# Kernel tuning notes

Measured on AMD Instinct MI355X. Metric: run time of the kernel, lower is better.

Reference implementation:

```python
import jax, jax.numpy as jnp
import numpy as np

N, L, H, E = 4, 4096, 8, 64
CHUNK = 128  # chunk size for the blocked causal scan
EPS = 1e-6


def elu_feature_map(x):
    # phi(x) = elu(x) + 1 (default feature map of fast-transformers)
    return jax.nn.elu(x) + 1.0


def causal_dot_product(Q, K, V, chunk=CHUNK):
    """out[n,l,h,:] = sum_{s<=l} (Q[n,l,h,:].K[n,s,h,:]) * V[n,s,h,:].
    Chunked scan over the [E,M] KV state: O(N L H E M) without an [L,L] matrix."""
    n, l, h, e = Q.shape
    m = V.shape[-1]
    nc = l // chunk

    def to_chunks(x):
        # [n, l, h, d] -> [nc, n, h, chunk, d]
        return x.reshape(n, nc, chunk, h, x.shape[-1]).transpose(1, 0, 3, 2, 4)

    q, k, v = to_chunks(Q), to_chunks(K), to_chunks(V)
    tril = jnp.tril(jnp.ones((chunk, chunk), dtype=Q.dtype))

    def step(S, xs):  # S: [n, h, e, m] running sum of k v^T
        qc, kc, vc = xs  # [n, h, chunk, e/m]
        inter = jnp.einsum('nhce,nhem->nhcm', qc, S)
        attn = jnp.einsum('nhce,nhde->nhcd', qc, kc) * tril  # intra-chunk causal
        intra = jnp.einsum('nhcd,nhdm->nhcm', attn, vc)
        S = S + jnp.einsum('nhce,nhcm->nhem', kc, vc)
        return S, inter + intra

    S0 = jnp.zeros((n, h, e, m), dtype=Q.dtype)
    _, out = jax.lax.scan(step, S0, (q, k, v))  # [nc, n, h, chunk, m]
    return out.transpose(1, 0, 3, 2, 4).reshape(n, l, h, m)


def setup_inputs() -> dict:
    key = jax.random.key(0)
    k1, k2, k3 = jax.random.split(key, 3)
    return {
        'queries': jax.random.normal(k1, (N, L, H, E), jnp.float32),
        'keys': jax.random.normal(k2, (N, L, H, E), jnp.float32),
        'values': jax.random.normal(k3, (N, L, H, E), jnp.float32),
        'key_lengths': jnp.ones((N, L), jnp.float32),  # float length mask
    }


def reference(queries, keys, values, key_lengths):
    Q = elu_feature_map(queries)
    K = elu_feature_map(keys) * key_lengths[:, :, None, None]
    # denominator: Z[n,l,h] = 1 / (Q[n,l,h] . cumsum_s<=l K[n,s,h] + eps)
    Z = 1.0 / (jnp.einsum('nlhe,nlhe->nlh', Q, jnp.cumsum(K, axis=1)) + EPS)
    V_new = causal_dot_product(Q, K, values)
    return V_new * Z[:, :, :, None]
```

## Files before the change

### kernel.cpp

```cpp
#include <hip/hip_runtime.h>
#include <math.h>

#define NN 4
#define LL 4096
#define HH 8
#define EE 64
#define CHK 64
#define GSUP 4
#define NSUP 16
#define NH (NN*HH)
#define NBLK (NH*NSUP)
#define NCH64 (LL/CHK)
#define EPSF 1e-6f

typedef float f32x4 __attribute__((ext_vector_type(4)));
typedef __bf16 bf16x8 __attribute__((ext_vector_type(8)));
typedef __bf16 bf16x4 __attribute__((ext_vector_type(4)));

__device__ __forceinline__ float phi_map(float x) {
  return x > 0.0f ? x + 1.0f : __expf(x);
}

#define MFMA(a, b, c) __builtin_amdgcn_mfma_f32_16x16x32_bf16((a), (b), (c), 0, 0, 0)

__device__ __forceinline__ int swz64(int row, int d) {
  return row * 64 + (d & 7) + 8 * ((d >> 3) ^ ((row >> 2) & 7));
}
__device__ __forceinline__ int frag64(int row, int blk) {
  return row * 64 + 8 * (blk ^ ((row >> 2) & 7));
}

#define K1_ISSUE(J, BUF) { \
  const int l0i = (sc * GSUP + (J)) * CHK; \
  _Pragma("unroll") for (int it = 0; it < 4; ++it) { \
    int f = t + 256 * it; int d = f >> 4; int c4 = (f & 15) << 2; \
    size_t gb = (((size_t)n * LL + (size_t)(l0i + d)) * HH + h) * EE + c4; \
    pk[BUF][it] = *(const float4*)(Kg + gb); \
    pv[BUF][it] = *(const float4*)(Vg + gb); \
    pl[BUF][it] = KLg[n * LL + l0i + d]; } }

#define K1_STAGE(BUF) { \
  _Pragma("unroll") for (int it = 0; it < 4; ++it) { \
    int f = t + 256 * it; int d = f >> 4; int c4 = (f & 15) << 2; \
    float klr = pl[BUF][it]; float4 kk = pk[BUF][it]; float4 vv = pv[BUF][it]; \
    float ka[4] = {phi_map(kk.x) * klr, phi_map(kk.y) * klr, phi_map(kk.z) * klr, phi_map(kk.w) * klr}; \
    float va[4] = {vv.x, vv.y, vv.z, vv.w}; \
    _Pragma("unroll") for (int jj = 0; jj < 4; ++jj) { \
      sKt[BUF][swz64(c4 + jj, d)] = (__bf16)ka[jj]; \
      sVt[BUF][swz64(c4 + jj, d)] = (__bf16)va[jj]; } } }

__global__ __launch_bounds__(256, 2) void k_chunksums(
    const float* __restrict__ Kg, const float* __restrict__ Vg,
    const float* __restrict__ KLg, __bf16* __restrict__ ScG, __bf16* __restrict__ KscG)
{
  __shared__ __bf16 sKt[2][4096];
  __shared__ __bf16 sVt[2][4096];
  const int g = blockIdx.x;
  const int sc = g & (NSUP - 1);
  const int nh = g >> 4;
  const int h = nh % HH;
  const int n = nh / HH;
  const int t = threadIdx.x;
  const int w = t >> 6;
  const int lane = t & 63;
  const int lg = lane >> 4;
  const int li = lane & 15;
  const int arow = 16 * w + li;

  float4 pk[2][4], pv[2][4];
  float pl[2][4];

  K1_ISSUE(0, 0);
  K1_STAGE(0);

  f32x4 acc[4];
  #pragma unroll
  for (int nt = 0; nt < 4; ++nt) acc[nt] = (f32x4){0.f, 0.f, 0.f, 0.f};

  bf16x8 ones;
  #pragma unroll
  for (int i = 0; i < 8; ++i) ones[i] = (__bf16)1.0f;

  #pragma unroll
  for (int j = 0; j < GSUP; ++j) {
    if (j + 1 < GSUP) K1_ISSUE(j + 1, (j + 1) & 1);
    __syncthreads();

    bf16x8 bV0 = *(const bf16x8*)&sVt[j & 1][frag64(arow, lg)];
    bf16x8 bV1 = *(const bf16x8*)&sVt[j & 1][frag64(arow, 4 + lg)];

    f32x4 accK[4];
    #pragma unroll
    for (int nt = 0; nt < 4; ++nt) accK[nt] = (f32x4){0.f, 0.f, 0.f, 0.f};

    #pragma unroll
    for (int nt = 0; nt < 4; ++nt) {
      bf16x8 a0 = *(const bf16x8*)&sKt[j & 1][frag64(li + 16 * nt, lg)];
      bf16x8 a1 = *(const bf16x8*)&sKt[j & 1][frag64(li + 16 * nt, 4 + lg)];
      acc[nt] = MFMA(a0, bV0, acc[nt]);
      acc[nt] = MFMA(a1, bV1, acc[nt]);
      if (w == 0) {
        accK[nt] = MFMA(ones, a0, accK[nt]);
        accK[nt] = MFMA(ones, a1, accK[nt]);
      }
    }
    if (w == 0 && lg == 0) {
      #pragma unroll
      for (int nt = 0; nt < 4; ++nt)
        KscG[(size_t)(g * GSUP + j) * 64 + li + 16 * nt] = (__bf16)accK[nt][0];
    }
    if (j + 1 < GSUP) K1_STAGE((j + 1) & 1);
  }

  __bf16* sp = ScG + (size_t)g * 4096;
  #pragma unroll
  for (int nt = 0; nt < 4; ++nt) {
    bf16x4 sv;
    #pragma unroll
    for (int reg = 0; reg < 4; ++reg) sv[reg] = (__bf16)acc[nt][reg];
    *(bf16x4*)(sp + arow * 64 + 16 * nt + 4 * lg) = sv;
  }
}

__global__ __launch_bounds__(256) void k_prefix(
    __bf16* __restrict__ Sc, __bf16* __restrict__ Ksc)
{
  const int bid = blockIdx.x;
  const int t = threadIdx.x;
  if (bid < NH * 16) {
    const int nh = bid >> 4;
    const int strip = bid & 15;
    const int entry = strip * 256 + t;
    __bf16 v[NSUP];
    #pragma unroll
    for (int c = 0; c < NSUP; ++c)
      v[c] = Sc[((size_t)(nh * NSUP + c) << 12) + entry];
    float run = 0.0f;
    #pragma unroll
    for (int c = 0; c < NSUP; ++c) {
      Sc[((size_t)(nh * NSUP + c) << 12) + entry] = (__bf16)run;
      run += (float)v[c];
    }
  } else {
    const int idx = (bid - NH * 16) * 256 + t;
    const int nh = idx >> 6;
    const int e = idx & 63;
    __bf16 v[NCH64];
    #pragma unroll
    for (int c = 0; c < NCH64; ++c)
      v[c] = Ksc[((size_t)(nh * NCH64 + c) << 6) + e];
    float run = 0.0f;
    #pragma unroll
    for (int c = 0; c < NCH64; ++c) {
      Ksc[((size_t)(nh * NCH64 + c) << 6) + e] = (__bf16)run;
      run += (float)v[c];
    }
  }
}

#define P2_ISSUE(CC) { \
  const int l0i = (sc * GSUP + (CC)) * CHK; \
  _Pragma("unroll") for (int it = 0; it < 4; ++it) { \
    int f = t + 256 * it; int d = f >> 4; int c4 = (f & 15) << 2; \
    size_t gb = (((size_t)n * LL + (size_t)(l0i + d)) * HH + h) * EE + c4; \
    pk[it] = *(const float4*)(Kg + gb); \
    pv[it] = *(const float4*)(Vg + gb); \
    pl[it] = KLg[n * LL + l0i + d]; } \
  { const float* qr = Qg + (((size_t)n * LL + (size_t)(l0i + arow)) * HH + h) * EE; \
    pq[0] = *(const float4*)(qr + 8 * lg); \
    pq[1] = *(const float4*)(qr + 8 * lg + 4); \
    pq[2] = *(const float4*)(qr + 32 + 8 * lg); \
    pq[3] = *(const float4*)(qr + 32 + 8 * lg + 4); } }

#define P2_STAGE(QB) { \
  _Pragma("unroll") for (int it = 0; it < 4; ++it) { \
    int f = t + 256 * it; int d = f >> 4; int c4 = (f & 15) << 2; \
    float klr = pl[it]; float4 kk = pk[it]; float4 vv = pv[it]; \
    float ka[4] = {phi_map(kk.x) * klr, phi_map(kk.y) * klr, phi_map(kk.z) * klr, phi_map(kk.w) * klr}; \
    float va[4] = {vv.x, vv.y, vv.z, vv.w}; \
    bf16x4 kv4; \
    kv4[0] = (__bf16)ka[0]; kv4[1] = (__bf16)ka[1]; kv4[2] = (__bf16)ka[2]; kv4[3] = (__bf16)ka[3]; \
    *(bf16x4*)&sKe[QB][d * 64 + 8 * ((c4 >> 3) ^ ((d >> 2) & 7)) + (c4 & 7)] = kv4; \
    _Pragma("unroll") for (int jj = 0; jj < 4; ++jj) { \
      sKt[QB][swz64(c4 + jj, d)] = (__bf16)ka[jj]; \
      sVt[QB][swz64(c4 + jj, d)] = (__bf16)va[jj]; } } \
  { float4 q0 = pq[0], q1 = pq[1], q2 = pq[2], q3 = pq[3]; \
    bf16x8 a0, a1; \
    a0[0] = (__bf16)phi_map(q0.x); a0[1] = (__bf16)phi_map(q0.y); \
    a0[2] = (__bf16)phi_map(q0.z); a0[3] = (__bf16)phi_map(q0.w); \
    a0[4] = (__bf16)phi_map(q1.x); a0[5] = (__bf16)phi_map(q1.y); \
    a0[6] = (__bf16)phi_map(q1.z); a0[7] = (__bf16)phi_map(q1.w); \
    a1[0] = (__bf16)phi_map(q2.x); a1[1] = (__bf16)phi_map(q2.y); \
    a1[2] = (__bf16)phi_map(q2.z); a1[3] = (__bf16)phi_map(q2.w); \
    a1[4] = (__bf16)phi_map(q3.x); a1[5] = (__bf16)phi_map(q3.y); \
    a1[6] = (__bf16)phi_map(q3.z); a1[7] = (__bf16)phi_map(q3.w); \
    aQ[QB][0] = a0; aQ[QB][1] = a1; } }

__global__ __launch_bounds__(256, 2) void k_pass2(
    const float* __restrict__ Qg, const float* __restrict__ Kg,
    const float* __restrict__ Vg, const float* __restrict__ KLg,
    const __bf16* __restrict__ Sp, const __bf16* __restrict__ Ksp,
    float* __restrict__ Og)
{
  __shared__ __bf16 sKe[2][4096];
  __shared__ __bf16 sKt[2][4096];
  __shared__ __bf16 sVt[2][4096];
  __shared__ __bf16 sU[2][4096];
  __shared__ __bf16 sP[4][1024];

  const int g = blockIdx.x;
  const int sc = g & (NSUP - 1);
  const int nh = g >> 4;
  const int h = nh % HH;
  const int n = nh / HH;
  const int t = threadIdx.x;
  const int w = t >> 6;
  const int lane = t & 63;
  const int lg = lane >> 4;
  const int li = lane & 15;
  const int arow = 16 * w + li;

  float4 pk[4], pv[4], pq[4];
  float pl[4];
  bf16x8 aQ[2][2];

  {
    const bf16x8* sp8 = (const bf16x8*)(Sp + (size_t)g * 4096);
    bf16x8 s0 = sp8[2 * t];
    bf16x8 s1 = sp8[2 * t + 1];
    int m = t >> 2, eb = (t & 3) * 2;
    *(bf16x8*)&sU[0][frag64(m, eb)] = s0;
    *(bf16x8*)&sU[0][frag64(m, eb + 1)] = s1;
  }

  f32x4 accS[4];
  #pragma unroll
  for (int nt = 0; nt < 4; ++nt) {
    bf16x4 sv = *(const bf16x4*)(Sp + (size_t)g * 4096 + arow * 64 + 16 * nt + 4 * lg);
    #pragma unroll
    for (int reg = 0; reg < 4; ++reg) accS[nt][reg] = (float)sv[reg];
  }

  P2_ISSUE(0);
  P2_STAGE(0);

  #pragma unroll
  for (int cc = 0; cc < GSUP; ++cc) {
    const int cb = cc & 1, nb = cb ^ 1;
    __syncthreads();

    if (cc + 1 < GSUP) P2_ISSUE(cc + 1);

    bf16x8 aQ0 = aQ[cb][0], aQ1 = aQ[cb][1];

    f32x4 acc[4];
    #pragma unroll
    for (int nt = 0; nt < 4; ++nt) {
      acc[nt] = (f32x4){0.f, 0.f, 0.f, 0.f};
      bf16x8 aS0 = *(const bf16x8*)&sU[cb][frag64(li + 16 * nt, lg)];
      bf16x8 aS1 = *(const bf16x8*)&sU[cb][frag64(li + 16 * nt, 4 + lg)];
      acc[nt] = MFMA(aS0, aQ0, acc[nt]);
      acc[nt] = MFMA(aS1, aQ1, acc[nt]);
    }

    const __bf16* kb = Ksp + (size_t)(g * GSUP + cc) * 64;
    bf16x8 ks0 = *(const bf16x8*)(kb + 8 * lg);
    bf16x8 ks1 = *(const bf16x8*)(kb + 32 + 8 * lg);
    float dv = 0.0f;
    #pragma unroll
    for (int i = 0; i < 8; ++i) {
      dv += (float)aQ0[i] * (float)ks0[i];
      dv += (float)aQ1[i] * (float)ks1[i];
    }
    dv += __shfl_xor(dv, 16);
    dv += __shfl_xor(dv, 32);

    f32x4 at2[4];
    #pragma unroll
    for (int nt = 0; nt < 4; ++nt) at2[nt] = (f32x4){0.f, 0.f, 0.f, 0.f};
    for (int nt = 0; nt <= w; ++nt) {
      bf16x8 aK0 = *(const bf16x8*)&sKe[cb][frag64(li + 16 * nt, lg)];
      bf16x8 aK1 = *(const bf16x8*)&sKe[cb][frag64(li + 16 * nt, 4 + lg)];
      at2[nt] = MFMA(aK0, aQ0, at2[nt]);
      at2[nt] = MFMA(aK1, aQ1, at2[nt]);
    }

    float rs = 0.0f;
    #pragma unroll
    for (int nt = 0; nt < 4; ++nt) {
      bf16x4 pw;
      #pragma unroll
      for (int reg = 0; reg < 4; ++reg) {
        int kk = 16 * nt + 4 * lg + reg;
        float av = (kk <= arow) ? at2[nt][reg] : 0.0f;
        rs += av;
        pw[reg] = (__bf16)av;
      }
      *(bf16x4*)&sP[w][li * 64 + 8 * ((2 * nt + (lg >> 1)) ^ (li & 7)) + 4 * (lg & 1)] = pw;
    }
    rs += __shfl_xor(rs, 16);
    rs += __shfl_xor(rs, 32);

    {
      bf16x8 bP0 = *(const bf16x8*)&sP[w][li * 64 + 8 * (lg ^ (li & 7))];
      bf16x8 bP1 = *(const bf16x8*)&sP[w][li * 64 + 8 * ((4 + lg) ^ (li & 7))];
      #pragma unroll
      for (int nt = 0; nt < 4; ++nt) {
        bf16x8 aV0 = *(const bf16x8*)&sVt[cb][frag64(li + 16 * nt, lg)];
        bf16x8 aV1 = *(const bf16x8*)&sVt[cb][frag64(li + 16 * nt, 4 + lg)];
        acc[nt] = MFMA(aV0, bP0, acc[nt]);
        acc[nt] = MFMA(aV1, bP1, acc[nt]);
      }
    }

    const int l0 = (sc * GSUP + cc) * CHK;
    {
      float inv = 1.0f / (dv + rs + EPSF);
      size_t ob = (((size_t)n * LL + (size_t)(l0 + arow)) * HH + h) * EE;
      #pragma unroll
      for (int nt = 0; nt < 4; ++nt) {
        float4 o = make_float4(acc[nt][0] * inv, acc[nt][1] * inv,
                               acc[nt][2] * inv, acc[nt][3] * inv);
        *(float4*)(Og + ob + 16 * nt + 4 * lg) = o;
      }
    }

    if (cc + 1 < GSUP) {
      bf16x8 bV0 = *(const bf16x8*)&sVt[cb][frag64(arow, lg)];
      bf16x8 bV1 = *(const bf16x8*)&sVt[cb][frag64(arow, 4 + lg)];
      #pragma unroll
      for (int nt = 0; nt < 4; ++nt) {
        bf16x8 aKt0 = *(const bf16x8*)&sKt[cb][frag64(li + 16 * nt, lg)];
        bf16x8 aKt1 = *(const bf16x8*)&sKt[cb][frag64(li + 16 * nt, 4 + lg)];
        accS[nt] = MFMA(aKt0, bV0, accS[nt]);
        accS[nt] = MFMA(aKt1, bV1, accS[nt]);
        bf16x4 sw;
        #pragma unroll
        for (int reg = 0; reg < 4; ++reg) sw[reg] = (__bf16)accS[nt][reg];
        *(bf16x4*)&sU[nb][arow * 64 + 8 * ((2 * nt + (lg >> 1)) ^ ((arow >> 2) & 7)) + 4 * (lg & 1)] = sw;
      }
      P2_STAGE(nb);
    }
  }
}

extern "C" void kernel_launch(void* const* d_in, const int* in_sizes, int n_in,
                              void* d_out, int out_size, void* d_ws, size_t ws_size,
                              hipStream_t stream) {
  const float* Qg  = (const float*)d_in[0];
  const float* Kg  = (const float*)d_in[1];
  const float* Vg  = (const float*)d_in[2];
  const float* KLg = (const float*)d_in[3];
  float* Og = (float*)d_out;

  __bf16* Sc  = (__bf16*)d_ws;
  __bf16* Ksc = (__bf16*)((char*)d_ws + (size_t)NBLK * 4096 * 2);

  hipLaunchKernelGGL(k_chunksums, dim3(NBLK), dim3(256), 0, stream, Kg, Vg, KLg, Sc, Ksc);
  hipLaunchKernelGGL(k_prefix, dim3(NH * 16 + 8), dim3(256), 0, stream, Sc, Ksc);
  hipLaunchKernelGGL(k_pass2, dim3(NBLK), dim3(256), 0, stream, Qg, Kg, Vg, KLg, Sc, Ksc, Og);
}
```

Before: 47.34 us.

## Warp-specialize pass2 into producer waves staging K/V and consumer waves computing

Launches pass2 with 512 threads. Waves 4-7 act as producers that load K, V and the length mask, apply the feature map and stage the next chunk into shared memory. Waves 0-3 do the MFMA compute and prefetch Q into registers. This replaces the old scheme where the same waves both prefetched into registers and computed, with the aim of overlapping global loads with compute and easing register pressure. The cost is one resident block per CU under the new launch bounds and half the threads sitting idle during each phase.

```diff
diff --git a/kernel.cpp b/kernel.cpp
--- a/kernel.cpp
+++ b/kernel.cpp
@@ -158,45 +158,7 @@
   }
 }
 
-#define P2_ISSUE(CC) { \
-  const int l0i = (sc * GSUP + (CC)) * CHK; \
-  _Pragma("unroll") for (int it = 0; it < 4; ++it) { \
-    int f = t + 256 * it; int d = f >> 4; int c4 = (f & 15) << 2; \
-    size_t gb = (((size_t)n * LL + (size_t)(l0i + d)) * HH + h) * EE + c4; \
-    pk[it] = *(const float4*)(Kg + gb); \
-    pv[it] = *(const float4*)(Vg + gb); \
-    pl[it] = KLg[n * LL + l0i + d]; } \
-  { const float* qr = Qg + (((size_t)n * LL + (size_t)(l0i + arow)) * HH + h) * EE; \
-    pq[0] = *(const float4*)(qr + 8 * lg); \
-    pq[1] = *(const float4*)(qr + 8 * lg + 4); \
-    pq[2] = *(const float4*)(qr + 32 + 8 * lg); \
-    pq[3] = *(const float4*)(qr + 32 + 8 * lg + 4); } }
-
-#define P2_STAGE(QB) { \
-  _Pragma("unroll") for (int it = 0; it < 4; ++it) { \
-    int f = t + 256 * it; int d = f >> 4; int c4 = (f & 15) << 2; \
-    float klr = pl[it]; float4 kk = pk[it]; float4 vv = pv[it]; \
-    float ka[4] = {phi_map(kk.x) * klr, phi_map(kk.y) * klr, phi_map(kk.z) * klr, phi_map(kk.w) * klr}; \
-    float va[4] = {vv.x, vv.y, vv.z, vv.w}; \
-    bf16x4 kv4; \
-    kv4[0] = (__bf16)ka[0]; kv4[1] = (__bf16)ka[1]; kv4[2] = (__bf16)ka[2]; kv4[3] = (__bf16)ka[3]; \
-    *(bf16x4*)&sKe[QB][d * 64 + 8 * ((c4 >> 3) ^ ((d >> 2) & 7)) + (c4 & 7)] = kv4; \
-    _Pragma("unroll") for (int jj = 0; jj < 4; ++jj) { \
-      sKt[QB][swz64(c4 + jj, d)] = (__bf16)ka[jj]; \
-      sVt[QB][swz64(c4 + jj, d)] = (__bf16)va[jj]; } } \
-  { float4 q0 = pq[0], q1 = pq[1], q2 = pq[2], q3 = pq[3]; \
-    bf16x8 a0, a1; \
-    a0[0] = (__bf16)phi_map(q0.x); a0[1] = (__bf16)phi_map(q0.y); \
-    a0[2] = (__bf16)phi_map(q0.z); a0[3] = (__bf16)phi_map(q0.w); \
-    a0[4] = (__bf16)phi_map(q1.x); a0[5] = (__bf16)phi_map(q1.y); \
-    a0[6] = (__bf16)phi_map(q1.z); a0[7] = (__bf16)phi_map(q1.w); \
-    a1[0] = (__bf16)phi_map(q2.x); a1[1] = (__bf16)phi_map(q2.y); \
-    a1[2] = (__bf16)phi_map(q2.z); a1[3] = (__bf16)phi_map(q2.w); \
-    a1[4] = (__bf16)phi_map(q3.x); a1[5] = (__bf16)phi_map(q3.y); \
-    a1[6] = (__bf16)phi_map(q3.z); a1[7] = (__bf16)phi_map(q3.w); \
-    aQ[QB][0] = a0; aQ[QB][1] = a1; } }
-
-__global__ __launch_bounds__(256, 2) void k_pass2(
+__global__ __launch_bounds__(512, 1) void k_pass2(
     const float* __restrict__ Qg, const float* __restrict__ Kg,
     const float* __restrict__ Vg, const float* __restrict__ KLg,
     const __bf16* __restrict__ Sp, const __bf16* __restrict__ Ksp,
@@ -218,129 +180,198 @@
   const int lane = t & 63;
   const int lg = lane >> 4;
   const int li = lane & 15;
-  const int arow = 16 * w + li;
-
-  float4 pk[4], pv[4], pq[4];
-  float pl[4];
-  bf16x8 aQ[2][2];
-
-  {
-    const bf16x8* sp8 = (const bf16x8*)(Sp + (size_t)g * 4096);
-    bf16x8 s0 = sp8[2 * t];
-    bf16x8 s1 = sp8[2 * t + 1];
-    int m = t >> 2, eb = (t & 3) * 2;
-    *(bf16x8*)&sU[0][frag64(m, eb)] = s0;
-    *(bf16x8*)&sU[0][frag64(m, eb + 1)] = s1;
-  }
+  const int cw = w & 3;
+  const int arow = 16 * cw + li;
+  const int t2 = t & 255;
 
   f32x4 accS[4];
-  #pragma unroll
-  for (int nt = 0; nt < 4; ++nt) {
-    bf16x4 sv = *(const bf16x4*)(Sp + (size_t)g * 4096 + arow * 64 + 16 * nt + 4 * lg);
-    #pragma unroll
-    for (int reg = 0; reg < 4; ++reg) accS[nt][reg] = (float)sv[reg];
-  }
-
-  P2_ISSUE(0);
-  P2_STAGE(0);
+  float4 pq[4];
+
+  if (w >= 4) {
+    const int l0i = sc * GSUP * CHK;
+    #pragma unroll
+    for (int it = 0; it < 4; ++it) {
+      int f = t2 + 256 * it; int d = f >> 4; int c4 = (f & 15) << 2;
+      size_t gb = (((size_t)n * LL + (size_t)(l0i + d)) * HH + h) * EE + c4;
+      float4 kk = *(const float4*)(Kg + gb);
+      float4 vv = *(const float4*)(Vg + gb);
+      float klr = KLg[n * LL + l0i + d];
+      float ka[4] = {phi_map(kk.x) * klr, phi_map(kk.y) * klr,
+                     phi_map(kk.z) * klr, phi_map(kk.w) * klr};
+      float va[4] = {vv.x, vv.y, vv.z, vv.w};
+      bf16x4 kv4;
+      kv4[0] = (__bf16)ka[0]; kv4[1] = (__bf16)ka[1];
+      kv4[2] = (__bf16)ka[2]; kv4[3] = (__bf16)ka[3];
+      *(bf16x4*)&sKe[0][d * 64 + 8 * ((c4 >> 3) ^ ((d >> 2) & 7)) + (c4 & 7)] = kv4;
+      #pragma unroll
+      for (int jj = 0; jj < 4; ++jj) {
+        sKt[0][swz64(c4 + jj, d)] = (__bf16)ka[jj];
+        sVt[0][swz64(c4 + jj, d)] = (__bf16)va[jj];
+      }
+    }
+  } else {
+    {
+      const bf16x8* sp8 = (const bf16x8*)(Sp + (size_t)g * 4096);
+      bf16x8 s0 = sp8[2 * t];
+      bf16x8 s1 = sp8[2 * t + 1];
+      int m = t >> 2, eb = (t & 3) * 2;
+      *(bf16x8*)&sU[0][frag64(m, eb)] = s0;
+      *(bf16x8*)&sU[0][frag64(m, eb + 1)] = s1;
+    }
+    #pragma unroll
+    for (int nt = 0; nt < 4; ++nt) {
+      bf16x4 sv = *(const bf16x4*)(Sp + (size_t)g * 4096 + arow * 64 + 16 * nt + 4 * lg);
+      #pragma unroll
+      for (int reg = 0; reg < 4; ++reg) accS[nt][reg] = (float)sv[reg];
+    }
+    {
+      const float* qr = Qg + (((size_t)n * LL + (size_t)(sc * GSUP * CHK + arow)) * HH + h) * EE;
+      pq[0] = *(const float4*)(qr + 8 * lg);
+      pq[1] = *(const float4*)(qr + 8 * lg + 4);
+      pq[2] = *(const float4*)(qr + 32 + 8 * lg);
+      pq[3] = *(const float4*)(qr + 32 + 8 * lg + 4);
+    }
+  }
+  __syncthreads();
 
   #pragma unroll
   for (int cc = 0; cc < GSUP; ++cc) {
     const int cb = cc & 1, nb = cb ^ 1;
+
+    if (w < 4) {
+      bf16x8 aQ0, aQ1;
+      {
+        float4 q0 = pq[0], q1 = pq[1], q2 = pq[2], q3 = pq[3];
+        aQ0[0] = (__bf16)phi_map(q0.x); aQ0[1] = (__bf16)phi_map(q0.y);
+        aQ0[2] = (__bf16)phi_map(q0.z); aQ0[3] = (__bf16)phi_map(q0.w);
+        aQ0[4] = (__bf16)phi_map(q1.x); aQ0[5] = (__bf16)phi_map(q1.y);
+        aQ0[6] = (__bf16)phi_map(q1.z); aQ0[7] = (__bf16)phi_map(q1.w);
+        aQ1[0] = (__bf16)phi_map(q2.x); aQ1[1] = (__bf16)phi_map(q2.y);
+        aQ1[2] = (__bf16)phi_map(q2.z); aQ1[3] = (__bf16)phi_map(q2.w);
+        aQ1[4] = (__bf16)phi_map(q3.x); aQ1[5] = (__bf16)phi_map(q3.y);
+        aQ1[6] = (__bf16)phi_map(q3.z); aQ1[7] = (__bf16)phi_map(q3.w);
+      }
+      if (cc + 1 < GSUP) {
+        const float* qr = Qg + (((size_t)n * LL +
+            (size_t)((sc * GSUP + cc + 1) * CHK + arow)) * HH + h) * EE;
+        pq[0] = *(const float4*)(qr + 8 * lg);
+        pq[1] = *(const float4*)(qr + 8 * lg + 4);
+        pq[2] = *(const float4*)(qr + 32 + 8 * lg);
+        pq[3] = *(const float4*)(qr + 32 + 8 * lg + 4);
+      }
+
+      const __bf16* kb = Ksp + (size_t)(g * GSUP + cc) * 64;
+      bf16x8 ks0 = *(const bf16x8*)(kb + 8 * lg);
+      bf16x8 ks1 = *(const bf16x8*)(kb + 32 + 8 * lg);
+
+      f32x4 acc[4];
+      #pragma unroll
+      for (int nt = 0; nt < 4; ++nt) {
+        acc[nt] = (f32x4){0.f, 0.f, 0.f, 0.f};
+        bf16x8 aS0 = *(const bf16x8*)&sU[cb][frag64(li + 16 * nt, lg)];
+        bf16x8 aS1 = *(const bf16x8*)&sU[cb][frag64(li + 16 * nt, 4 + lg)];
+        acc[nt] = MFMA(aS0, aQ0, acc[nt]);
+        acc[nt] = MFMA(aS1, aQ1, acc[nt]);
+      }
+
+      float dv = 0.0f;
+      #pragma unroll
+      for (int i = 0; i < 8; ++i) {
+        dv += (float)aQ0[i] * (float)ks0[i];
+        dv += (float)aQ1[i] * (float)ks1[i];
+      }
+      dv += __shfl_xor(dv, 16);
+      dv += __shfl_xor(dv, 32);
+
+      f32x4 at2[4];
+      #pragma unroll
+      for (int nt = 0; nt < 4; ++nt) at2[nt] = (f32x4){0.f, 0.f, 0.f, 0.f};
+      for (int nt = 0; nt <= cw; ++nt) {
+        bf16x8 aK0 = *(const bf16x8*)&sKe[cb][frag64(li + 16 * nt, lg)];
+        bf16x8 aK1 = *(const bf16x8*)&sKe[cb][frag64(li + 16 * nt, 4 + lg)];
+        at2[nt] = MFMA(aK0, aQ0, at2[nt]);
+        at2[nt] = MFMA(aK1, aQ1, at2[nt]);
+      }
+
+      float rs = 0.0f;
+      #pragma unroll
+      for (int nt = 0; nt < 4; ++nt) {
+        bf16x4 pw;
+        #pragma unroll
+        for (int reg = 0; reg < 4; ++reg) {
+          int kk = 16 * nt + 4 * lg + reg;
+          float av = (kk <= arow) ? at2[nt][reg] : 0.0f;
+          rs += av;
+          pw[reg] = (__bf16)av;
+        }
+        *(bf16x4*)&sP[cw][li * 64 + 8 * ((2 * nt + (lg >> 1)) ^ (li & 7)) + 4 * (lg & 1)] = pw;
+      }
+      rs += __shfl_xor(rs, 16);
+      rs += __shfl_xor(rs, 32);
+
+      {
+        bf16x8 bP0 = *(const bf16x8*)&sP[cw][li * 64 + 8 * (lg ^ (li & 7))];
+        bf16x8 bP1 = *(const bf16x8*)&sP[cw][li * 64 + 8 * ((4 + lg) ^ (li & 7))];
+        #pragma unroll
+        for (int nt = 0; nt < 4; ++nt) {
+          bf16x8 aV0 = *(const bf16x8*)&sVt[cb][frag64(li + 16 * nt, lg)];
+          bf16x8 aV1 = *(const bf16x8*)&sVt[cb][frag64(li + 16 * nt, 4 + lg)];
+          acc[nt] = MFMA(aV0, bP0, acc[nt]);
+          acc[nt] = MFMA(aV1, bP1, acc[nt]);
+        }
+      }
+
+      const int l0 = (sc * GSUP + cc) * CHK;
+      {
+        float inv = 1.0f / (dv + rs + EPSF);
+        size_t ob = (((size_t)n * LL + (size_t)(l0 + arow)) * HH + h) * EE;
+        #pragma unroll
+        for (int nt = 0; nt < 4; ++nt) {
+          float4 o = make_float4(acc[nt][0] * inv, acc[nt][1] * inv,
+                                 acc[nt][2] * inv, acc[nt][3] * inv);
+          *(float4*)(Og + ob + 16 * nt + 4 * lg) = o;
+        }
+      }
+
+      if (cc + 1 < GSUP) {
+        bf16x8 bV0 = *(const bf16x8*)&sVt[cb][frag64(arow, lg)];
+        bf16x8 bV1 = *(const bf16x8*)&sVt[cb][frag64(arow, 4 + lg)];
+        #pragma unroll
+        for (int nt = 0; nt < 4; ++nt) {
+          bf16x8 aKt0 = *(const bf16x8*)&sKt[cb][frag64(li + 16 * nt, lg)];
+          bf16x8 aKt1 = *(const bf16x8*)&sKt[cb][frag64(li + 16 * nt, 4 + lg)];
+          accS[nt] = MFMA(aKt0, bV0, accS[nt]);
+          accS[nt] = MFMA(aKt1, bV1, accS[nt]);
+          bf16x4 sw;
+          #pragma unroll
+          for (int reg = 0; reg < 4; ++reg) sw[reg] = (__bf16)accS[nt][reg];
+          *(bf16x4*)&sU[nb][arow * 64 + 8 * ((2 * nt + (lg >> 1)) ^ ((arow >> 2) & 7)) + 4 * (lg & 1)] = sw;
+        }
+      }
+    } else if (cc + 1 < GSUP) {
+      const int l0i = (sc * GSUP + cc + 1) * CHK;
+      #pragma unroll
+      for (int it = 0; it < 4; ++it) {
+        int f = t2 + 256 * it; int d = f >> 4; int c4 = (f & 15) << 2;
+        size_t gb = (((size_t)n * LL + (size_t)(l0i + d)) * HH + h) * EE + c4;
+        float4 kk = *(const float4*)(Kg + gb);
+        float4 vv = *(const float4*)(Vg + gb);
+        float klr = KLg[n * LL + l0i + d];
+        float ka[4] = {phi_map(kk.x) * klr, phi_map(kk.y) * klr,
+                       phi_map(kk.z) * klr, phi_map(kk.w) * klr};
+        float va[4] = {vv.x, vv.y, vv.z, vv.w};
+        bf16x4 kv4;
+        kv4[0] = (__bf16)ka[0]; kv4[1] = (__bf16)ka[1];
+        kv4[2] = (__bf16)ka[2]; kv4[3] = (__bf16)ka[3];
+        *(bf16x4*)&sKe[nb][d * 64 + 8 * ((c4 >> 3) ^ ((d >> 2) & 7)) + (c4 & 7)] = kv4;
+        #pragma unroll
+        for (int jj = 0; jj < 4; ++jj) {
+          sKt[nb][swz64(c4 + jj, d)] = (__bf16)ka[jj];
+          sVt[nb][swz64(c4 + jj, d)] = (__bf16)va[jj];
+        }
+      }
+    }
     __syncthreads();
-
-    if (cc + 1 < GSUP) P2_ISSUE(cc + 1);
-
-    bf16x8 aQ0 = aQ[cb][0], aQ1 = aQ[cb][1];
-
-    f32x4 acc[4];
-    #pragma unroll
-    for (int nt = 0; nt < 4; ++nt) {
-      acc[nt] = (f32x4){0.f, 0.f, 0.f, 0.f};
-      bf16x8 aS0 = *(const bf16x8*)&sU[cb][frag64(li + 16 * nt, lg)];
-      bf16x8 aS1 = *(const bf16x8*)&sU[cb][frag64(li + 16 * nt, 4 + lg)];
-      acc[nt] = MFMA(aS0, aQ0, acc[nt]);
-      acc[nt] = MFMA(aS1, aQ1, acc[nt]);
-    }
-
-    const __bf16* kb = Ksp + (size_t)(g * GSUP + cc) * 64;
-    bf16x8 ks0 = *(const bf16x8*)(kb + 8 * lg);
-    bf16x8 ks1 = *(const bf16x8*)(kb + 32 + 8 * lg);
-    float dv = 0.0f;
-    #pragma unroll
-    for (int i = 0; i < 8; ++i) {
-      dv += (float)aQ0[i] * (float)ks0[i];
-      dv += (float)aQ1[i] * (float)ks1[i];
-    }
-    dv += __shfl_xor(dv, 16);
-    dv += __shfl_xor(dv, 32);
-
-    f32x4 at2[4];
-    #pragma unroll
-    for (int nt = 0; nt < 4; ++nt) at2[nt] = (f32x4){0.f, 0.f, 0.f, 0.f};
-    for (int nt = 0; nt <= w; ++nt) {
-      bf16x8 aK0 = *(const bf16x8*)&sKe[cb][frag64(li + 16 * nt, lg)];
-      bf16x8 aK1 = *(const bf16x8*)&sKe[cb][frag64(li + 16 * nt, 4 + lg)];
-      at2[nt] = MFMA(aK0, aQ0, at2[nt]);
-      at2[nt] = MFMA(aK1, aQ1, at2[nt]);
-    }
-
-    float rs = 0.0f;
-    #pragma unroll
-    for (int nt = 0; nt < 4; ++nt) {
-      bf16x4 pw;
-      #pragma unroll
-      for (int reg = 0; reg < 4; ++reg) {
-        int kk = 16 * nt + 4 * lg + reg;
-        float av = (kk <= arow) ? at2[nt][reg] : 0.0f;
-        rs += av;
-        pw[reg] = (__bf16)av;
-      }
-      *(bf16x4*)&sP[w][li * 64 + 8 * ((2 * nt + (lg >> 1)) ^ (li & 7)) + 4 * (lg & 1)] = pw;
-    }
-    rs += __shfl_xor(rs, 16);
-    rs += __shfl_xor(rs, 32);
-
-    {
-      bf16x8 bP0 = *(const bf16x8*)&sP[w][li * 64 + 8 * (lg ^ (li & 7))];
-      bf16x8 bP1 = *(const bf16x8*)&sP[w][li * 64 + 8 * ((4 + lg) ^ (li & 7))];
-      #pragma unroll
-      for (int nt = 0; nt < 4; ++nt) {
-        bf16x8 aV0 = *(const bf16x8*)&sVt[cb][frag64(li + 16 * nt, lg)];
-        bf16x8 aV1 = *(const bf16x8*)&sVt[cb][frag64(li + 16 * nt, 4 + lg)];
-        acc[nt] = MFMA(aV0, bP0, acc[nt]);
-        acc[nt] = MFMA(aV1, bP1, acc[nt]);
-      }
-    }
-
-    const int l0 = (sc * GSUP + cc) * CHK;
-    {
-      float inv = 1.0f / (dv + rs + EPSF);
-      size_t ob = (((size_t)n * LL + (size_t)(l0 + arow)) * HH + h) * EE;
-      #pragma unroll
-      for (int nt = 0; nt < 4; ++nt) {
-        float4 o = make_float4(acc[nt][0] * inv, acc[nt][1] * inv,
-                               acc[nt][2] * inv, acc[nt][3] * inv);
-        *(float4*)(Og + ob + 16 * nt + 4 * lg) = o;
-      }
-    }
-
-    if (cc + 1 < GSUP) {
-      bf16x8 bV0 = *(const bf16x8*)&sVt[cb][frag64(arow, lg)];
-      bf16x8 bV1 = *(const bf16x8*)&sVt[cb][frag64(arow, 4 + lg)];
-      #pragma unroll
-      for (int nt = 0; nt < 4; ++nt) {
-        bf16x8 aKt0 = *(const bf16x8*)&sKt[cb][frag64(li + 16 * nt, lg)];
-        bf16x8 aKt1 = *(const bf16x8*)&sKt[cb][frag64(li + 16 * nt, 4 + lg)];
-        accS[nt] = MFMA(aKt0, bV0, accS[nt]);
-        accS[nt] = MFMA(aKt1, bV1, accS[nt]);
-        bf16x4 sw;
-        #pragma unroll
-        for (int reg = 0; reg < 4; ++reg) sw[reg] = (__bf16)accS[nt][reg];
-        *(bf16x4*)&sU[nb][arow * 64 + 8 * ((2 * nt + (lg >> 1)) ^ ((arow >> 2) & 7)) + 4 * (lg & 1)] = sw;
-      }
-      P2_STAGE(nb);
-    }
   }
 }
 
@@ -358,5 +389,5 @@
 
   hipLaunchKernelGGL(k_chunksums, dim3(NBLK), dim3(256), 0, stream, Kg, Vg, KLg, Sc, Ksc);
   hipLaunchKernelGGL(k_prefix, dim3(NH * 16 + 8), dim3(256), 0, stream, Sc, Ksc);
-  hipLaunchKernelGGL(k_pass2, dim3(NBLK), dim3(256), 0, stream, Qg, Kg, Vg, KLg, Sc, Ksc, Og);
-}
+  hipLaunchKernelGGL(k_pass2, dim3(NBLK), dim3(512), 0, stream, Qg, Kg, Vg, KLg, Sc, Ksc, Og);
+}
```

Result: slower. 50.49 us (+6.7%).
